# Kernel tuning notes

Measured on AMD Instinct MI355X. Metric: run time of the kernel, lower is better.

Reference implementation:

```python
import jax, jax.numpy as jnp
import numpy as np

EMBED_DIMS = 256

def setup_inputs() -> dict:
    key = jax.random.key(0)
    ks = jax.random.split(key, 6)
    C = EMBED_DIMS
    x = jax.random.normal(ks[0], (4, 2048, C), dtype=jnp.float32)
    prev_x = jax.random.normal(ks[1], (4, 2048, C), dtype=jnp.float32)
    s = 1.0 / np.sqrt(C)
    W_qkv = jax.random.uniform(ks[2], (C, 3 * C), dtype=jnp.float32, minval=-s, maxval=s)
    b_qkv = jax.random.uniform(ks[3], (3 * C,), dtype=jnp.float32, minval=-s, maxval=s)
    W_out = jax.random.uniform(ks[4], (C, C), dtype=jnp.float32, minval=-s, maxval=s)
    b_out = jax.random.uniform(ks[5], (C,), dtype=jnp.float32, minval=-s, maxval=s)
    return {"x": x, "prev_x": prev_x, "W_qkv": W_qkv, "b_qkv": b_qkv,
            "W_out": W_out, "b_out": b_out}

def reference(x, prev_x, W_qkv, b_qkv, W_out, b_out):
    B, N, C = x.shape
    xx = jnp.concatenate([prev_x, x], axis=1)          # [B, S, C], S = 2N
    qkv = xx @ W_qkv + b_qkv                            # [B, S, 3C]
    q, k, v = jnp.split(qkv, 3, axis=-1)                # each [B, S, C]
    scale = 1.0 / jnp.sqrt(jnp.asarray(C, dtype=x.dtype))
    attn = jax.nn.softmax(jnp.einsum('bqc,bkc->bqk', q, k) * scale, axis=-1)
    out = jnp.einsum('bqk,bkc->bqc', attn, v)           # [B, S, C]
    out = out @ W_out + b_out
    return out[:, -N:, :]                               # [B, N, C]
```

## Files before the change

### kernel.cpp

```cpp
#include <hip/hip_runtime.h>

typedef __bf16 bf16;
typedef __attribute__((ext_vector_type(8))) __bf16 bf16x8;
typedef __attribute__((ext_vector_type(4))) __bf16 bf16x4;
typedef __attribute__((ext_vector_type(4))) float f32x4;
typedef __attribute__((ext_vector_type(16))) float f32x16;
typedef __attribute__((ext_vector_type(4))) unsigned u32x4;

#define MFMA16(a, b, c) __builtin_amdgcn_mfma_f32_16x16x32_bf16(a, b, c, 0, 0, 0)
#define MFMA32(a, b, c) __builtin_amdgcn_mfma_f32_32x32x16_bf16(a, b, c, 0, 0, 0)

__device__ inline void gload_lds16(const void* g, void* l) {
  __builtin_amdgcn_global_load_lds(
      (const __attribute__((address_space(1))) void*)g,
      (__attribute__((address_space(3))) void*)l, 16, 0, 0);
}

__device__ inline unsigned packbf(float a, float b) {
  unsigned short x = __builtin_bit_cast(unsigned short, (bf16)a);
  unsigned short y = __builtin_bit_cast(unsigned short, (bf16)b);
  return (unsigned)x | ((unsigned)y << 16);
}

__global__ __launch_bounds__(256) void prep_kernel(
    const float* __restrict__ x, const float* __restrict__ px,
    const float* __restrict__ Wqkv, const float* __restrict__ Wout,
    bf16* __restrict__ Xbf, bf16* __restrict__ Wqkvt, bf16* __restrict__ Woutt)
{
  int tid = blockIdx.x * 256 + threadIdx.x;
  int nth = gridDim.x * 256;
  for (int i = tid; i < (4 * 4096 * 256) / 4; i += nth) {
    int e = i << 2;
    int b = e >> 20;
    int r = e & 1048575;
    const float* src = (r < 524288) ? (px + (b << 19) + r)
                                    : (x + (b << 19) + (r - 524288));
    float4 f = *(const float4*)src;
    bf16x4 o = { (bf16)f.x, (bf16)f.y, (bf16)f.z, (bf16)f.w };
    *(bf16x4*)(Xbf + e) = o;
  }
  for (int i = tid; i < 768 * 256; i += nth) {
    int n = i >> 8, k = i & 255;
    Wqkvt[i] = (bf16)Wqkv[k * 768 + n];
  }
  for (int i = tid; i < 256 * 256; i += nth) {
    int n = i >> 8, k = i & 255;
    Woutt[i] = (bf16)Wout[k * 256 + n];
  }
}

template<int MODE>
__global__ __launch_bounds__(256) void gemm_kernel(
    const bf16* __restrict__ A, const bf16* __restrict__ Wt,
    const float* __restrict__ bias,
    bf16* __restrict__ Qo, bf16* __restrict__ KVo, float* __restrict__ Fo)
{
  const int bm = blockIdx.x * 64;
  const int n0 = blockIdx.y * 128;
  const int tid = threadIdx.x;
  const int lane = tid & 63, w = tid >> 6;
  const int l15 = lane & 15, lg = lane >> 4;

  alignas(16) __shared__ bf16 Alds[64 * 32];
  alignas(16) __shared__ bf16 Wlds[128 * 32];

  f32x4 acc[8] = {};

  for (int k0 = 0; k0 < 256; k0 += 32) {
    __syncthreads();
    {
      int c = tid;
      int row = c >> 2, kc = (c & 3) << 3;
      bf16x8 v = *(const bf16x8*)(A + (size_t)(bm + row) * 256 + k0 + kc);
      *(bf16x8*)((char*)Alds + ((c << 4) ^ (((row >> 1) & 3) << 4))) = v;
    }
    #pragma unroll
    for (int it = 0; it < 2; it++) {
      int c = it * 256 + tid;
      int row = c >> 2, kc = (c & 3) << 3;
      bf16x8 v = *(const bf16x8*)(Wt + (size_t)(n0 + row) * 256 + k0 + kc);
      *(bf16x8*)((char*)Wlds + ((c << 4) ^ (((row >> 1) & 3) << 4))) = v;
    }
    __syncthreads();
    const int arow = w * 16 + l15;
    bf16x8 afr = *(const bf16x8*)((char*)Alds +
        (((arow << 6) + (lg << 4)) ^ (((arow >> 1) & 3) << 4)));
    #pragma unroll
    for (int nt = 0; nt < 8; nt++) {
      const int wrow = nt * 16 + l15;
      bf16x8 bfr = *(const bf16x8*)((char*)Wlds +
          (((wrow << 6) + (lg << 4)) ^ (((wrow >> 1) & 3) << 4)));
      acc[nt] = MFMA16(afr, bfr, acc[nt]);
    }
  }

  #pragma unroll
  for (int nt = 0; nt < 8; nt++) {
    const int n = n0 + nt * 16 + l15;
    const float bv = bias[n];
    const int m0 = bm + w * 16 + lg * 4;
    if (MODE == 0) {
      const int bq = m0 >> 12;
      const int s = m0 & 4095;
      if (n < 256) {
        if (s >= 2048) {
          const int ks = n >> 4, h2 = (n >> 3) & 1, e = n & 7;
          #pragma unroll
          for (int r = 0; r < 4; r++) {
            const int qrow = bq * 2048 + (s - 2048) + r;
            Qo[(size_t)(qrow >> 5) * 8192 + ks * 512 +
               ((qrow & 31) + 32 * h2) * 8 + e] =
                (bf16)((acc[nt][r] + bv) * 0.0625f);
          }
        }
      } else if (n < 512) {
        const int d = n - 256;
        const int ks = d >> 4, h2 = (d >> 3) & 1, e = d & 7;
        const size_t tb = (size_t)(bq * 128 + (s >> 5)) * 16384;
        #pragma unroll
        for (int r = 0; r < 4; r++)
          KVo[tb + ks * 512 + (((s & 31) + r) + 32 * h2) * 8 + e] =
              (bf16)(acc[nt][r] + bv);
      } else {
        const int d = n - 512;
        const int kv32 = s & 31;
        const int sidx = kv32 >> 4, h2 = (kv32 >> 3) & 1, e0 = kv32 & 7;
        bf16x4 st = { (bf16)(acc[nt][0] + bv), (bf16)(acc[nt][1] + bv),
                      (bf16)(acc[nt][2] + bv), (bf16)(acc[nt][3] + bv) };
        *(bf16x4*)(KVo + (size_t)(bq * 128 + (s >> 5)) * 16384 + 8192 +
                   (sidx * 8 + (d >> 5)) * 512 + ((d & 31) + 32 * h2) * 8 + e0) = st;
      }
    } else {
      #pragma unroll
      for (int r = 0; r < 4; r++)
        Fo[(size_t)((m0 + r) * 256 + n)] = acc[nt][r] + bv;
    }
  }
}

__global__ __launch_bounds__(256, 2) void attn_kernel(
    const bf16* __restrict__ Qp, const bf16* __restrict__ KVp,
    bf16* __restrict__ Opart, float* __restrict__ ml)
{
  const int id = blockIdx.x;
  const int c = id & 7;
  const int b = (id >> 3) & 3;
  const int qb = id >> 5;
  const int tid = threadIdx.x;
  const int lane = tid & 63, w = tid >> 6;
  const int l31 = lane & 31, hi = lane >> 5;

  __shared__ bf16 lds[2][16384];

  const int qg = b * 64 + qb * 4 + w;
  const bf16* qbase = Qp + (size_t)qg * 8192 + lane * 8;
  bf16x8 qf[16];
  #pragma unroll
  for (int ks = 0; ks < 16; ks++)
    qf[ks] = *(const bf16x8*)(qbase + ks * 512);

  const bf16* kvtile0 = KVp + (size_t)(b * 128 + c * 16) * 16384;

  auto stage = [&](int t) {
    const char* g = (const char*)(kvtile0 + (size_t)t * 16384) + w * 8192 + lane * 16;
    char* l = (char*)&lds[t & 1][0] + w * 8192;
    #pragma unroll
    for (int j = 0; j < 8; j++)
      gload_lds16(g + j * 1024, l + j * 1024);
  };
  stage(0);

  f32x16 o[8] = {};
  float m_run = -1e30f, l_run = 0.f;

  for (int t = 0; t < 16; t++) {
    __syncthreads();
    if (t + 1 < 16) stage(t + 1);
    const bf16* kbuf = &lds[t & 1][0];
    const bf16* vbuf = kbuf + 8192;

    f32x16 p = {};
    __builtin_amdgcn_s_setprio(1);
    #pragma unroll
    for (int ks = 0; ks < 16; ks++) {
      bf16x8 kf = *(const bf16x8*)(kbuf + ks * 512 + lane * 8);
      p = MFMA32(kf, qf[ks], p);
    }
    __builtin_amdgcn_s_setprio(0);

    float mt = fmaxf(p[0], p[1]);
    #pragma unroll
    for (int i = 2; i < 16; i++) mt = fmaxf(mt, p[i]);
    mt = fmaxf(mt, __shfl_xor(mt, 32));
    if (!__all(mt <= m_run + 8.f)) {
      const float m_new = fmaxf(m_run, mt);
      const float alpha = __expf(m_run - m_new);
      l_run *= alpha;
      #pragma unroll
      for (int i = 0; i < 8; i++)
        #pragma unroll
        for (int j = 0; j < 16; j++) o[i][j] *= alpha;
      m_run = m_new;
    }
    float ps = 0.f;
    #pragma unroll
    for (int i = 0; i < 16; i++) { p[i] = __expf(p[i] - m_run); ps += p[i]; }
    ps += __shfl_xor(ps, 32);
    l_run += ps;

    unsigned u[8], xp[8];
    #pragma unroll
    for (int i = 0; i < 8; i++) u[i] = packbf(p[2 * i], p[2 * i + 1]);
    #pragma unroll
    for (int i = 0; i < 8; i++)
      xp[i] = (unsigned)__shfl_xor((int)u[i], 32);
    const u32x4 w0 = hi ? (u32x4){xp[2], xp[3], u[2], u[3]}
                        : (u32x4){u[0], u[1], xp[0], xp[1]};
    const u32x4 w1 = hi ? (u32x4){xp[6], xp[7], u[6], u[7]}
                        : (u32x4){u[4], u[5], xp[4], xp[5]};
    const bf16x8 pf0 = __builtin_bit_cast(bf16x8, w0);
    const bf16x8 pf1 = __builtin_bit_cast(bf16x8, w1);

    __builtin_amdgcn_s_setprio(1);
    #pragma unroll
    for (int dg = 0; dg < 8; dg++) {
      bf16x8 v0 = *(const bf16x8*)(vbuf + dg * 512 + lane * 8);
      o[dg] = MFMA32(v0, pf0, o[dg]);
      bf16x8 v1 = *(const bf16x8*)(vbuf + (8 + dg) * 512 + lane * 8);
      o[dg] = MFMA32(v1, pf1, o[dg]);
    }
    __builtin_amdgcn_s_setprio(0);
  }

  const int q = b * 2048 + qb * 128 + w * 32 + l31;
  bf16* ob = Opart + ((size_t)c * 8192 + q) * 256;
  #pragma unroll
  for (int dg = 0; dg < 8; dg++) {
    #pragma unroll
    for (int r4 = 0; r4 < 4; r4++) {
      const int d = dg * 32 + r4 * 8 + hi * 4;
      bf16x4 st = { (bf16)o[dg][r4 * 4 + 0], (bf16)o[dg][r4 * 4 + 1],
                    (bf16)o[dg][r4 * 4 + 2], (bf16)o[dg][r4 * 4 + 3] };
      *(bf16x4*)(ob + d) = st;
    }
  }
  if (hi == 0) {
    float2 v = { m_run, l_run };
    *(float2*)(ml + ((size_t)c * 8192 + q) * 2) = v;
  }
}

__global__ __launch_bounds__(256) void combine_kernel(
    const bf16* __restrict__ Opart, const float* __restrict__ ml,
    bf16* __restrict__ AO)
{
  const int id = blockIdx.x * 256 + threadIdx.x;
  const int q = id >> 5, dc = (id & 31) << 3;
  float ms[8], ls[8], M = -1e30f;
  #pragma unroll
  for (int s = 0; s < 8; s++) {
    float2 v = *(const float2*)(ml + ((size_t)s * 8192 + q) * 2);
    ms[s] = v.x; ls[s] = v.y;
    M = fmaxf(M, v.x);
  }
  float L = 0.f;
  float acc[8] = {};
  #pragma unroll
  for (int s = 0; s < 8; s++) {
    const float wgt = __expf(ms[s] - M);
    L += ls[s] * wgt;
    bf16x8 v = *(const bf16x8*)(Opart + ((size_t)s * 8192 + q) * 256 + dc);
    #pragma unroll
    for (int j = 0; j < 8; j++) acc[j] += wgt * (float)v[j];
  }
  const float inv = 1.f / L;
  bf16x8 st;
  #pragma unroll
  for (int j = 0; j < 8; j++) st[j] = (bf16)(acc[j] * inv);
  *(bf16x8*)(AO + (size_t)q * 256 + dc) = st;
}

extern "C" void kernel_launch(void* const* d_in, const int* in_sizes, int n_in,
                              void* d_out, int out_size, void* d_ws, size_t ws_size,
                              hipStream_t stream) {
  const float* x    = (const float*)d_in[0];
  const float* px   = (const float*)d_in[1];
  const float* Wqkv = (const float*)d_in[2];
  const float* bqkv = (const float*)d_in[3];
  const float* Wout = (const float*)d_in[4];
  const float* bout = (const float*)d_in[5];
  float* out = (float*)d_out;

  char* ws = (char*)d_ws;
  bf16* Qp    = (bf16*)(ws);
  bf16* KVp   = (bf16*)(ws + 4194304);
  bf16* Woutt = (bf16*)(ws + 20971520);
  bf16* Wqkvt = (bf16*)(ws + 21102592);
  float* ml   = (float*)(ws + 21495808);
  bf16* Xbf   = (bf16*)(ws + 22020096);
  bf16* Opart = (bf16*)(ws + 22020096);
  bf16* AObf  = (bf16*)(ws);

  prep_kernel<<<dim3(512), dim3(256), 0, stream>>>(x, px, Wqkv, Wout,
                                                   Xbf, Wqkvt, Woutt);
  gemm_kernel<0><<<dim3(256, 6), dim3(256), 0, stream>>>(
      Xbf, Wqkvt, bqkv, Qp, KVp, nullptr);
  attn_kernel<<<dim3(512), dim3(256), 0, stream>>>(Qp, KVp, Opart, ml);
  combine_kernel<<<dim3(1024), dim3(256), 0, stream>>>(Opart, ml, AObf);
  gemm_kernel<1><<<dim3(128, 2), dim3(256), 0, stream>>>(
      AObf, Woutt, bout, nullptr, nullptr, out);
}
```

Before: 96.17 us.

## Software-pipeline QK of next tile with softmax/PV of current tile

Splits K and V staging into separate LDS rings (triple-buffered K, double-buffered V) so the QK^T MFMAs for tile t+1 can be issued before the softmax and PV of tile t, overlapping matrix work with the exp/reduction phase. Max and sum reductions are also rewritten as trees to shorten dependency chains, and the loop is fully unrolled. This raises register pressure (an extra f32x16 of scores live) and LDS use, which may affect occupancy at 2 blocks per CU.

```diff
diff --git a/kernel.cpp b/kernel.cpp
--- a/kernel.cpp
+++ b/kernel.cpp
@@ -150,7 +150,8 @@
   const int lane = tid & 63, w = tid >> 6;
   const int l31 = lane & 31, hi = lane >> 5;
 
-  __shared__ bf16 lds[2][16384];
+  __shared__ bf16 Kb[3][8192];
+  __shared__ bf16 Vb[2][8192];
 
   const int qg = b * 64 + qb * 4 + w;
   const bf16* qbase = Qp + (size_t)qg * 8192 + lane * 8;
@@ -159,26 +160,24 @@
   for (int ks = 0; ks < 16; ks++)
     qf[ks] = *(const bf16x8*)(qbase + ks * 512);
 
-  const bf16* kvtile0 = KVp + (size_t)(b * 128 + c * 16) * 16384;
-
-  auto stage = [&](int t) {
-    const char* g = (const char*)(kvtile0 + (size_t)t * 16384) + w * 8192 + lane * 16;
-    char* l = (char*)&lds[t & 1][0] + w * 8192;
-    #pragma unroll
-    for (int j = 0; j < 8; j++)
+  const char* kvtile0 = (const char*)(KVp + (size_t)(b * 128 + c * 16) * 16384);
+
+  auto stage_K = [&](int t, int ring) {
+    const char* g = kvtile0 + (size_t)t * 32768 + w * 4096 + lane * 16;
+    char* l = (char*)&Kb[ring][0] + w * 4096;
+    #pragma unroll
+    for (int j = 0; j < 4; j++)
       gload_lds16(g + j * 1024, l + j * 1024);
   };
-  stage(0);
-
-  f32x16 o[8] = {};
-  float m_run = -1e30f, l_run = 0.f;
-
-  for (int t = 0; t < 16; t++) {
-    __syncthreads();
-    if (t + 1 < 16) stage(t + 1);
-    const bf16* kbuf = &lds[t & 1][0];
-    const bf16* vbuf = kbuf + 8192;
-
+  auto stage_V = [&](int t, int ring) {
+    const char* g = kvtile0 + (size_t)t * 32768 + 16384 + w * 4096 + lane * 16;
+    char* l = (char*)&Vb[ring][0] + w * 4096;
+    #pragma unroll
+    for (int j = 0; j < 4; j++)
+      gload_lds16(g + j * 1024, l + j * 1024);
+  };
+
+  auto qk = [&](const bf16* kbuf) {
     f32x16 p = {};
     __builtin_amdgcn_s_setprio(1);
     #pragma unroll
@@ -187,10 +186,34 @@
       p = MFMA32(kf, qf[ks], p);
     }
     __builtin_amdgcn_s_setprio(0);
-
-    float mt = fmaxf(p[0], p[1]);
-    #pragma unroll
-    for (int i = 2; i < 16; i++) mt = fmaxf(mt, p[i]);
+    return p;
+  };
+
+  stage_K(0, 0);
+  stage_V(0, 0);
+  stage_K(1, 1);
+
+  f32x16 o[8] = {};
+  f32x16 pA;
+  float m_run = -1e30f, l_run = 0.f;
+
+  #pragma unroll
+  for (int t = 0; t < 16; t++) {
+    __syncthreads();
+    if (t + 2 < 16) stage_K(t + 2, (t + 2) % 3);
+    if (t + 1 < 16) stage_V(t + 1, (t + 1) & 1);
+
+    if (t == 0) pA = qk(&Kb[0][0]);
+    f32x16 pN = {};
+    if (t + 1 < 16) pN = qk(&Kb[(t + 1) % 3][0]);
+
+    f32x16 p = pA;
+    float m0 = fmaxf(p[0], p[1]),   m1 = fmaxf(p[2], p[3]);
+    float m2 = fmaxf(p[4], p[5]),   m3 = fmaxf(p[6], p[7]);
+    float m4 = fmaxf(p[8], p[9]),   m5 = fmaxf(p[10], p[11]);
+    float m6 = fmaxf(p[12], p[13]), m7 = fmaxf(p[14], p[15]);
+    m0 = fmaxf(m0, m1); m2 = fmaxf(m2, m3); m4 = fmaxf(m4, m5); m6 = fmaxf(m6, m7);
+    float mt = fmaxf(fmaxf(m0, m2), fmaxf(m4, m6));
     mt = fmaxf(mt, __shfl_xor(mt, 32));
     if (!__all(mt <= m_run + 8.f)) {
       const float m_new = fmaxf(m_run, mt);
@@ -202,9 +225,13 @@
         for (int j = 0; j < 16; j++) o[i][j] *= alpha;
       m_run = m_new;
     }
-    float ps = 0.f;
-    #pragma unroll
-    for (int i = 0; i < 16; i++) { p[i] = __expf(p[i] - m_run); ps += p[i]; }
+    #pragma unroll
+    for (int i = 0; i < 16; i++) p[i] = __expf(p[i] - m_run);
+    float s0 = (p[0] + p[1]) + (p[2] + p[3]);
+    float s1 = (p[4] + p[5]) + (p[6] + p[7]);
+    float s2 = (p[8] + p[9]) + (p[10] + p[11]);
+    float s3 = (p[12] + p[13]) + (p[14] + p[15]);
+    float ps = (s0 + s1) + (s2 + s3);
     ps += __shfl_xor(ps, 32);
     l_run += ps;
 
@@ -221,6 +248,7 @@
     const bf16x8 pf0 = __builtin_bit_cast(bf16x8, w0);
     const bf16x8 pf1 = __builtin_bit_cast(bf16x8, w1);
 
+    const bf16* vbuf = &Vb[t & 1][0];
     __builtin_amdgcn_s_setprio(1);
     #pragma unroll
     for (int dg = 0; dg < 8; dg++) {
@@ -230,6 +258,8 @@
       o[dg] = MFMA32(v1, pf1, o[dg]);
     }
     __builtin_amdgcn_s_setprio(0);
+
+    pA = pN;
   }
 
   const int q = b * 2048 + qb * 128 + w * 32 + l31;
```

Result: no change. 97.63 us (+1.5%).
